# Optimization experiments

Hardware: AMD Instinct MI355X
Metric: run time of the kernel (lower is better)

## Reference

```python
import jax, jax.numpy as jnp
import numpy as np

NODES = 81
NODE_DIM = 2
IN_DIM = NODES * NODE_DIM  # 162
D = 256
H = 16
HD = D // H
DFF = 2048
T, B, E = 1024, 8, 648


def _layernorm(x, w, b, eps=1e-5):
    m = x.mean(-1, keepdims=True)
    v = x.var(-1, keepdims=True)
    return (x - m) / jnp.sqrt(v + eps) * w + b


def setup_inputs() -> dict:
    key = jax.random.key(0)
    ks = jax.random.split(key, 12)
    s = 0.02
    W = lambda k, shape: jax.random.normal(k, shape, jnp.float32) * s
    return {
        "src": jax.random.normal(ks[0], (T, B, IN_DIM), jnp.float32),
        "edge_index": jax.random.randint(ks[1], (2, E), 0, NODES),
        "gcn_w": W(ks[2], (NODE_DIM, NODE_DIM)),
        "gcn_b": jnp.zeros((NODE_DIM,), jnp.float32),
        "fc_w": W(ks[3], (IN_DIM, D)),
        "fc_b": jnp.zeros((D,), jnp.float32),
        "wq": W(ks[4], (D, D)), "bq": jnp.zeros((D,), jnp.float32),
        "wk": W(ks[5], (D, D)), "bk": jnp.zeros((D,), jnp.float32),
        "wv": W(ks[6], (D, D)), "bv": jnp.zeros((D,), jnp.float32),
        "wo": W(ks[7], (D, D)), "bo": jnp.zeros((D,), jnp.float32),
        "ln1_w": jnp.ones((D,), jnp.float32), "ln1_b": jnp.zeros((D,), jnp.float32),
        "ffn_w1": W(ks[8], (D, DFF)), "ffn_b1": jnp.zeros((DFF,), jnp.float32),
        "ffn_w2": W(ks[9], (DFF, D)), "ffn_b2": jnp.zeros((D,), jnp.float32),
        "ln2_w": jnp.ones((D,), jnp.float32), "ln2_b": jnp.zeros((D,), jnp.float32),
        "dec_w": W(ks[10], (D, IN_DIM)), "dec_b": jnp.zeros((IN_DIM,), jnp.float32),
    }


def reference(src, edge_index, gcn_w, gcn_b, fc_w, fc_b, wq, bq, wk, bk, wv, bv,
              wo, bo, ln1_w, ln1_b, ffn_w1, ffn_b1, ffn_w2, ffn_b2, ln2_w, ln2_b,
              dec_w, dec_b):
    t, b, _ = src.shape
    # ---- batched GCNConv(2,2): all T*B tiny graphs share one adjacency ----
    # src[t,b] = [in_flow(81), out_flow(81)] -> node features [81, 2]
    xg = jnp.swapaxes(src.reshape(t, b, NODE_DIM, NODES), -1, -2)  # [T,B,81,2]
    row, col = edge_index[0], edge_index[1]
    A = jnp.zeros((NODES, NODES), src.dtype).at[col, row].add(1.0)
    A = A + jnp.eye(NODES, dtype=src.dtype)          # add self-loops
    deg = A.sum(1)
    dinv = jnp.where(deg > 0, 1.0 / jnp.sqrt(deg), 0.0)
    A_hat = dinv[:, None] * A * dinv[None, :]        # D^-1/2 (A+I) D^-1/2
    hg = jnp.einsum('ij,tbjc->tbic', A_hat, xg @ gcn_w) + gcn_b  # [T,B,81,2]
    # gcn_output.transpose(0,1).view(-1): channel-major flatten
    src2 = jnp.swapaxes(hg, -1, -2).reshape(t, b, IN_DIM)
    # ---- fc + positional encoding ----
    x = src2 @ fc_w + fc_b  # [T,B,D]
    pos = jnp.arange(t, dtype=jnp.float32)[:, None]
    div = jnp.exp(jnp.arange(0, D, 2, dtype=jnp.float32) * (-np.log(10000.0) / D))
    pe = jnp.zeros((t, D), x.dtype).at[:, 0::2].set(jnp.sin(pos * div))
    pe = pe.at[:, 1::2].set(jnp.cos(pos * div))
    x = x + pe[:, None, :]
    # ---- TransformerEncoderLayer (post-norm, relu, causal mask, eval) ----
    q = (x @ wq + bq).reshape(t, b, H, HD)
    k = (x @ wk + bk).reshape(t, b, H, HD)
    v = (x @ wv + bv).reshape(t, b, H, HD)
    scores = jnp.einsum('tbhd,sbhd->bhts', q, k) / jnp.sqrt(jnp.asarray(HD, x.dtype))
    causal = jnp.tril(jnp.ones((t, t), bool))
    scores = jnp.where(causal, scores, jnp.finfo(x.dtype).min)
    attn = jax.nn.softmax(scores, axis=-1)
    ctx = jnp.einsum('bhts,sbhd->tbhd', attn, v).reshape(t, b, D) @ wo + bo
    x = _layernorm(x + ctx, ln1_w, ln1_b)
    ff = jax.nn.relu(x @ ffn_w1 + ffn_b1) @ ffn_w2 + ffn_b2
    x = _layernorm(x + ff, ln2_w, ln2_b)
    return x @ dec_w + dec_b  # [T,B,162]
```

## Files before the change

kernel.cpp:

```cpp
#include <hip/hip_runtime.h>
#include <math.h>

#define T_    1024
#define B_    8
#define D_    256
#define H_    16
#define HD_   16
#define DFF_  2048
#define NODES_ 81
#define INDIM_ 162
#define E_    648
#define M_    (T_*B_)

typedef __bf16 bf16x8 __attribute__((ext_vector_type(8)));
typedef float  f32x4  __attribute__((ext_vector_type(4)));
typedef unsigned short ushort_t;
typedef unsigned int   uint_t;

__device__ __forceinline__ ushort_t f2bf(float f) {
    union { float f; uint_t u; } c; c.f = f;
    uint_t u = c.u;
    uint_t r = u + 0x7fffu + ((u >> 16) & 1u);
    return (ushort_t)(r >> 16);
}

__device__ __forceinline__ bf16x8 zero8() {
    bf16x8 v;
#pragma unroll
    for (int e = 0; e < 8; e++) v[e] = (__bf16)0.0f;
    return v;
}

__device__ __forceinline__ void gload_lds16(const void* g, void* l) {
    __builtin_amdgcn_global_load_lds(
        (const __attribute__((address_space(1))) void*)g,
        (__attribute__((address_space(3))) void*)l, 16, 0, 0);
}

__global__ __launch_bounds__(256) void build_weff_fused(
        const int* __restrict__ edge, const float* __restrict__ gcn_w,
        const float* __restrict__ gcn_b, const float* __restrict__ fc_w,
        const float* __restrict__ fc_b, ushort_t* __restrict__ weffT,
        float* __restrict__ beff) {
    __shared__ float A[NODES_ * NODES_];
    __shared__ float dinv[NODES_];
    int tid = threadIdx.x;
    for (int i = tid; i < NODES_ * NODES_; i += 256) A[i] = 0.f;
    __syncthreads();
    for (int e = tid; e < E_; e += 256) {
        int r = edge[e];
        int c = edge[E_ + e];
        atomicAdd(&A[c * NODES_ + r], 1.0f);
    }
    __syncthreads();
    if (tid < NODES_) A[tid * NODES_ + tid] += 1.0f;
    __syncthreads();
    if (tid < NODES_) {
        float s = 0.f;
        for (int k = 0; k < NODES_; k++) s += A[tid * NODES_ + k];
        dinv[tid] = (s > 0.f) ? rsqrtf(s) : 0.f;
    }
    __syncthreads();

    int d = tid;
    int j = blockIdx.x;
    if (j < NODES_) {
        float s0 = 0.f, s1 = 0.f;
        for (int i = 0; i < NODES_; i++) {
            float a = dinv[i] * A[i * NODES_ + j] * dinv[j];
            s0 += a * fc_w[(0 * NODES_ + i) * D_ + d];
            s1 += a * fc_w[(1 * NODES_ + i) * D_ + d];
        }
        weffT[d * 192 + j]          = f2bf(gcn_w[0] * s0 + gcn_w[1] * s1);
        weffT[d * 192 + NODES_ + j] = f2bf(gcn_w[2] * s0 + gcn_w[3] * s1);
    } else {
        float t0 = 0.f, t1 = 0.f;
        for (int i = 0; i < NODES_; i++) {
            t0 += fc_w[(0 * NODES_ + i) * D_ + d];
            t1 += fc_w[(1 * NODES_ + i) * D_ + d];
        }
        beff[d] = fc_b[d] + gcn_b[0] * t0 + gcn_b[1] * t1;
        for (int c = INDIM_; c < 192; c++) weffT[d * 192 + c] = 0;
    }
}

__device__ __forceinline__ void trans_tile(
        const float* __restrict__ in, ushort_t* __restrict__ out,
        int K, int N, int Kp, int Np, int bx, int by) {
    __shared__ float tile[32][33];
    int k0 = bx * 32, n0 = by * 32;
    int tx = threadIdx.x & 31, ty = threadIdx.x >> 5;
#pragma unroll
    for (int i = 0; i < 4; i++) {
        int r = k0 + ty + i * 8, c = n0 + tx;
        tile[ty + i * 8][tx] = (r < K && c < N) ? in[(size_t)r * N + c] : 0.f;
    }
    __syncthreads();
#pragma unroll
    for (int i = 0; i < 4; i++) {
        int r = n0 + ty + i * 8, c = k0 + tx;
        out[(size_t)r * Kp + c] = f2bf(tile[tx][ty + i * 8]);
    }
}

__global__ __launch_bounds__(256) void prep_all(
        const float* __restrict__ wq, const float* __restrict__ wk,
        const float* __restrict__ wv, const float* __restrict__ wo,
        const float* __restrict__ dec_w, const float* __restrict__ w1,
        const float* __restrict__ w2,
        const float* __restrict__ bq, const float* __restrict__ bk,
        const float* __restrict__ bv,
        ushort_t* __restrict__ wqkvT, ushort_t* __restrict__ woT,
        ushort_t* __restrict__ dwT, ushort_t* __restrict__ w1T,
        ushort_t* __restrict__ w2T, float* __restrict__ qkvbias) {
    int bid = blockIdx.x;
    if (bid < 64)        { int l = bid;        trans_tile(wq,   wqkvT,          D_,   D_,     D_,   D_,   l & 7,  l >> 3); }
    else if (bid < 128)  { int l = bid - 64;   trans_tile(wk,   wqkvT + 65536,  D_,   D_,     D_,   D_,   l & 7,  l >> 3); }
    else if (bid < 192)  { int l = bid - 128;  trans_tile(wv,   wqkvT + 131072, D_,   D_,     D_,   D_,   l & 7,  l >> 3); }
    else if (bid < 256)  { int l = bid - 192;  trans_tile(wo,   woT,            D_,   D_,     D_,   D_,   l & 7,  l >> 3); }
    else if (bid < 320)  { int l = bid - 256;  trans_tile(dec_w, dwT,           D_,   INDIM_, D_,   D_,   l & 7,  l >> 3); }
    else if (bid < 832)  { int l = bid - 320;  trans_tile(w1,   w1T,            D_,   DFF_,   D_,   DFF_, l & 7,  l >> 3); }
    else if (bid < 1344) { int l = bid - 832;  trans_tile(w2,   w2T,            DFF_, D_,     DFF_, D_,   l & 63, l >> 6); }
    else {
        int i = (bid - 1344) * 256 + threadIdx.x;
        if (i < 768) qkvbias[i] = (i < 256) ? bq[i] : ((i < 512) ? bk[i - 256] : bv[i - 512]);
    }
}

__global__ void src_to_bf16(const float* __restrict__ src, ushort_t* __restrict__ out) {
    int r = blockIdx.x, c = threadIdx.x;
    out[(size_t)r * 192 + c] = (c < INDIM_) ? f2bf(src[(size_t)r * INDIM_ + c]) : (ushort_t)0;
}

enum { EP_PE = 0, EP_QKV = 1, EP_PLAIN = 2, EP_RELU = 3, EP_DEC = 4, EP_PART = 5 };

template <int EPI, int TM, int KS>
__global__ __launch_bounds__(256) void gemm_bf16(
        const ushort_t* __restrict__ A, const ushort_t* __restrict__ BT,
        const float* __restrict__ bias, float* __restrict__ Cf,
        ushort_t* __restrict__ Cb, int M, int N, int K) {
    __shared__ ushort_t sA[TM * 64];
    __shared__ ushort_t sB[128 * 64];
    int tid = threadIdx.x;
    int w = tid >> 6, lane = tid & 63;
    int cc = lane & 15, q = lane >> 4;
    int bm = blockIdx.y * TM, bn = blockIdx.x * 128;
    int part = (KS > 1) ? blockIdx.z : 0;
    int kbeg = part * (K / KS), kend = kbeg + K / KS;

    int srow = (lane >> 3);
    int sslot = lane & 7;

    const int NJ = (TM == 128) ? 4 : 2;
    int mbase = (TM == 128) ? ((w >> 1) * 64) : 0;
    int nbase = (TM == 128) ? ((w & 1) * 64) : (w * 32);

    f32x4 acc[4][NJ];
#pragma unroll
    for (int i = 0; i < 4; i++)
#pragma unroll
        for (int j = 0; j < NJ; j++)
#pragma unroll
            for (int e = 0; e < 4; e++) acc[i][j][e] = 0.f;

    for (int k0 = kbeg; k0 < kend; k0 += 64) {
        if (TM == 128) {
#pragma unroll
            for (int i = 0; i < 4; i++) {
                int r = w * 32 + i * 8 + srow;
                const ushort_t* ga = A + (size_t)(bm + r) * K + k0 + ((sslot ^ (r & 7)) * 8);
                gload_lds16(ga, &sA[(w * 32 + i * 8) * 64]);
            }
        } else {
#pragma unroll
            for (int i = 0; i < 2; i++) {
                int r = w * 16 + i * 8 + srow;
                const ushort_t* ga = A + (size_t)(bm + r) * K + k0 + ((sslot ^ (r & 7)) * 8);
                gload_lds16(ga, &sA[(w * 16 + i * 8) * 64]);
            }
        }
#pragma unroll
        for (int i = 0; i < 4; i++) {
            int r = w * 32 + i * 8 + srow;
            const ushort_t* gb = BT + (size_t)(bn + r) * K + k0 + ((sslot ^ (r & 7)) * 8);
            gload_lds16(gb, &sB[(w * 32 + i * 8) * 64]);
        }
        __syncthreads();
#pragma unroll
        for (int ks = 0; ks < 2; ks++) {
            bf16x8 af[4], bfr[NJ];
#pragma unroll
            for (int i = 0; i < 4; i++) {
                int m = mbase + i * 16 + cc;
                int off = m * 64 + (((ks * 4 + q) ^ (cc & 7)) * 8);
                af[i] = *(const bf16x8*)&sA[off];
            }
#pragma unroll
            for (int j = 0; j < NJ; j++) {
                int n = nbase + j * 16 + cc;
                int off = n * 64 + (((ks * 4 + q) ^ (cc & 7)) * 8);
                bfr[j] = *(const bf16x8*)&sB[off];
            }
#pragma unroll
            for (int i = 0; i < 4; i++)
#pragma unroll
                for (int j = 0; j < NJ; j++)
                    acc[i][j] = __builtin_amdgcn_mfma_f32_16x16x32_bf16(af[i], bfr[j], acc[i][j], 0, 0, 0);
        }
        __syncthreads();
    }

#pragma unroll
    for (int i = 0; i < 4; i++) {
#pragma unroll
        for (int j = 0; j < NJ; j++) {
            int col = bn + nbase + j * 16 + cc;
            float bv = 0.f;
            if (EPI == EP_DEC) bv = (col < INDIM_) ? bias[col] : 0.f;
            else if (EPI != EP_PART) bv = bias[col];
#pragma unroll
            for (int reg = 0; reg < 4; reg++) {
                int row = bm + mbase + i * 16 + q * 4 + reg;
                float v = acc[i][j][reg] + bv;
                if (EPI == EP_PE) {
                    int t = row >> 3;
                    float freq = __expf((float)(col & ~1) * (-9.210340371976184f / 256.f));
                    float ang = (float)t * freq;
                    v += (col & 1) ? __cosf(ang) : __sinf(ang);
                    Cf[(size_t)row * N + col] = v;
                    Cb[(size_t)row * N + col] = f2bf(v);
                } else if (EPI == EP_QKV) {
                    int t = row >> 3, b = row & 7;
                    int nn = col & 255, which = col >> 8;
                    int h = nn >> 4, hd = nn & 15;
                    Cb[(size_t)which * 2097152 +
                       ((size_t)((b * H_ + h) * T_ + t)) * HD_ + hd] = f2bf(v);
                } else if (EPI == EP_PLAIN) {
                    Cf[(size_t)row * N + col] = v;
                } else if (EPI == EP_RELU) {
                    v = fmaxf(v, 0.f);
                    Cb[(size_t)row * N + col] = f2bf(v);
                } else if (EPI == EP_DEC) {
                    if (col < INDIM_) Cf[(size_t)row * INDIM_ + col] = v;
                } else if (EPI == EP_PART) {
                    Cf[(size_t)part * M * N + (size_t)row * N + col] = v;
                }
            }
        }
    }
}

__global__ __launch_bounds__(256) void attn_mfma(
        const ushort_t* __restrict__ Qb, const ushort_t* __restrict__ Kb,
        const ushort_t* __restrict__ Vb, ushort_t* __restrict__ ctxb) {
    int qc = 7 - blockIdx.x;
    int bh = blockIdx.y;
    int tid = threadIdx.x;
    int w = tid >> 6, lane = tid & 63;
    int cc = lane & 15, q = lane >> 4;
    int qb0 = qc * 128;

    __shared__ ushort_t Ks[64 * 24];
    __shared__ ushort_t VTs[16 * 72];
    __shared__ ushort_t Ps[4][32 * 72];

    const ushort_t* Qp = Qb + (size_t)bh * (T_ * HD_);
    const ushort_t* Kp = Kb + (size_t)bh * (T_ * HD_);
    const ushort_t* Vp = Vb + (size_t)bh * (T_ * HD_);

    bf16x8 qf[2];
#pragma unroll
    for (int i = 0; i < 2; i++) {
        if (q < 2)
            qf[i] = *(const bf16x8*)&Qp[(size_t)(qb0 + w * 32 + i * 16 + cc) * HD_ + q * 8];
        else
            qf[i] = zero8();
    }

    bf16x8 ones;
#pragma unroll
    for (int e = 0; e < 8; e++) ones[e] = (__bf16)1.0f;

    f32x4 ot[2], ls[2];
#pragma unroll
    for (int i = 0; i < 2; i++)
#pragma unroll
        for (int e = 0; e < 4; e++) { ot[i][e] = 0.f; ls[i][e] = 0.f; }

    int ntiles = 2 * (qc + 1);
    int qmaxw = qb0 + w * 32 + 31;

    for (int kb = 0; kb < ntiles; kb++) {
        __syncthreads();
        if (tid < 128) {
            int r = tid >> 1, half = tid & 1;
            *(bf16x8*)&Ks[r * 24 + half * 8] =
                *(const bf16x8*)&Kp[(size_t)(kb * 64 + r) * HD_ + half * 8];
        } else {
            int t2 = tid - 128;
            int r = t2 >> 1, half = t2 & 1;
            bf16x8 vv = *(const bf16x8*)&Vp[(size_t)(kb * 64 + r) * HD_ + half * 8];
#pragma unroll
            for (int e = 0; e < 8; e++)
                VTs[(half * 8 + e) * 72 + r] = ((const ushort_t*)&vv)[e];
        }
        __syncthreads();
        if (kb * 64 > qmaxw) continue;

        f32x4 s[2][4];
#pragma unroll
        for (int j = 0; j < 4; j++) {
            bf16x8 kf;
            if (q < 2) kf = *(const bf16x8*)&Ks[(j * 16 + cc) * 24 + q * 8];
            else kf = zero8();
#pragma unroll
            for (int i = 0; i < 2; i++) {
                f32x4 z;
#pragma unroll
                for (int e = 0; e < 4; e++) z[e] = 0.f;
                s[i][j] = __builtin_amdgcn_mfma_f32_16x16x32_bf16(qf[i], kf, z, 0, 0, 0);
            }
        }

#pragma unroll
        for (int i = 0; i < 2; i++) {
            int qrow0 = qb0 + w * 32 + i * 16 + q * 4;
            bool needmask = (kb * 64 + 63) > (qb0 + w * 32 + i * 16);
#pragma unroll
            for (int j = 0; j < 4; j++) {
                int key = kb * 64 + j * 16 + cc;
#pragma unroll
                for (int reg = 0; reg < 4; reg++) {
                    float p = __expf(s[i][j][reg] * 0.25f);
                    if (needmask && key > qrow0 + reg) p = 0.f;
                    union { float f; uint_t u; } cv; cv.f = p;
                    Ps[w][(i * 16 + q * 4 + reg) * 72 + j * 16 + cc] =
                        (ushort_t)(cv.u >> 16);
                }
            }
        }

#pragma unroll
        for (int kk = 0; kk < 2; kk++) {
            bf16x8 vf = *(const bf16x8*)&VTs[cc * 72 + kk * 32 + q * 8];
#pragma unroll
            for (int i = 0; i < 2; i++) {
                bf16x8 pf = *(const bf16x8*)&Ps[w][(i * 16 + cc) * 72 + kk * 32 + q * 8];
                ot[i] = __builtin_amdgcn_mfma_f32_16x16x32_bf16(vf, pf, ot[i], 0, 0, 0);
                ls[i] = __builtin_amdgcn_mfma_f32_16x16x32_bf16(ones, pf, ls[i], 0, 0, 0);
            }
        }
    }

    int b = bh >> 4, h = bh & 15;
#pragma unroll
    for (int i = 0; i < 2; i++) {
        int t = qb0 + w * 32 + i * 16 + cc;
        float linv = 1.f / ls[i][0];
        ushort_t* op = ctxb + ((size_t)t * B_ + b) * D_ + h * HD_ + q * 4;
#pragma unroll
        for (int reg = 0; reg < 4; reg++)
            op[reg] = f2bf(ot[i][reg] * linv);
    }
}

template <int NP, bool HASB>
__global__ __launch_bounds__(256) void ln_kernel(
        const float* __restrict__ X, const float* __restrict__ P0,
        const float* __restrict__ P1, const float* __restrict__ RB,
        const float* __restrict__ w, const float* __restrict__ b,
        float* __restrict__ out, ushort_t* __restrict__ outb) {
    int wv = threadIdx.x >> 6, lane = threadIdx.x & 63;
    int row = blockIdx.x * 4 + wv;
    int c = lane * 4;
    const float4 x4 = *(const float4*)&X[(size_t)row * D_ + c];
    const float4 p4 = *(const float4*)&P0[(size_t)row * D_ + c];
    float v0 = x4.x + p4.x, v1 = x4.y + p4.y, v2 = x4.z + p4.z, v3 = x4.w + p4.w;
    if (NP == 2) {
        const float4 q4 = *(const float4*)&P1[(size_t)row * D_ + c];
        v0 += q4.x; v1 += q4.y; v2 += q4.z; v3 += q4.w;
    }
    if (HASB) {
        const float4 r4 = *(const float4*)&RB[c];
        v0 += r4.x; v1 += r4.y; v2 += r4.z; v3 += r4.w;
    }
    float s  = v0 + v1 + v2 + v3;
    float sq = v0 * v0 + v1 * v1 + v2 * v2 + v3 * v3;
    for (int off = 32; off; off >>= 1) {
        s  += __shfl_xor(s, off);
        sq += __shfl_xor(sq, off);
    }
    float mean = s * (1.f / 256.f);
    float var  = sq * (1.f / 256.f) - mean * mean;
    float rstd = rsqrtf(var + 1e-5f);
    float o0 = (v0 - mean) * rstd * w[c + 0] + b[c + 0];
    float o1 = (v1 - mean) * rstd * w[c + 1] + b[c + 1];
    float o2 = (v2 - mean) * rstd * w[c + 2] + b[c + 2];
    float o3 = (v3 - mean) * rstd * w[c + 3] + b[c + 3];
    float4 o; o.x = o0; o.y = o1; o.z = o2; o.w = o3;
    *(float4*)&out[(size_t)row * D_ + c] = o;
    ushort4 ob;
    ob.x = f2bf(o0); ob.y = f2bf(o1); ob.z = f2bf(o2); ob.w = f2bf(o3);
    *(ushort4*)&outb[(size_t)row * D_ + c] = ob;
}

extern "C" void kernel_launch(void* const* d_in, const int* in_sizes, int n_in,
                              void* d_out, int out_size, void* d_ws, size_t ws_size,
                              hipStream_t stream) {
    (void)in_sizes; (void)n_in; (void)out_size; (void)ws_size;
    const float* src     = (const float*)d_in[0];
    const int*   edge    = (const int*)d_in[1];
    const float* gcn_w   = (const float*)d_in[2];
    const float* gcn_b   = (const float*)d_in[3];
    const float* fc_w    = (const float*)d_in[4];
    const float* fc_b    = (const float*)d_in[5];
    const float* wq      = (const float*)d_in[6];
    const float* bq      = (const float*)d_in[7];
    const float* wk      = (const float*)d_in[8];
    const float* bk      = (const float*)d_in[9];
    const float* wv      = (const float*)d_in[10];
    const float* bv      = (const float*)d_in[11];
    const float* wo      = (const float*)d_in[12];
    const float* bo      = (const float*)d_in[13];
    const float* ln1_w   = (const float*)d_in[14];
    const float* ln1_b   = (const float*)d_in[15];
    const float* ffn_w1  = (const float*)d_in[16];
    const float* ffn_b1  = (const float*)d_in[17];
    const float* ffn_w2  = (const float*)d_in[18];
    const float* ffn_b2  = (const float*)d_in[19];
    const float* ln2_w   = (const float*)d_in[20];
    const float* ln2_b   = (const float*)d_in[21];
    const float* dec_w   = (const float*)d_in[22];
    const float* dec_b   = (const float*)d_in[23];
    float* out = (float*)d_out;

    float* ws = (float*)d_ws;
    float* beff    = ws;
    float* qkvbias = ws + 256;
    float* x0      = ws + 1024;
    float* tmp     = x0  + 2097152;
    float* tmp2    = tmp + 2097152;
    float* x1      = tmp2 + 2097152;
    float* x2s     = x1  + 2097152;
    ushort_t* ub   = (ushort_t*)(ws + 10486784);
    ushort_t* srcb = ub;
    ushort_t* x0b  = ub + 1572864;
    ushort_t* x1b  = x0b + 2097152;
    ushort_t* x2b  = x1b + 2097152;
    ushort_t* ctxb = x2b + 2097152;
    ushort_t* hb   = ctxb + 2097152;
    ushort_t* qkvb = hb + 16777216;
    ushort_t* weffT= qkvb + 6291456;
    ushort_t* wqkvT= weffT + 49152;
    ushort_t* woT  = wqkvT + 196608;
    ushort_t* w1T  = woT + 65536;
    ushort_t* w2T  = w1T + 524288;
    ushort_t* dwT  = w2T + 524288;

    build_weff_fused<<<82, 256, 0, stream>>>(edge, gcn_w, gcn_b, fc_w, fc_b, weffT, beff);
    prep_all<<<1347, 256, 0, stream>>>(wq, wk, wv, wo, dec_w, ffn_w1, ffn_w2,
                                       bq, bk, bv, wqkvT, woT, dwT, w1T, w2T, qkvbias);
    src_to_bf16<<<8192, 192, 0, stream>>>(src, srcb);

    gemm_bf16<EP_PE, 64, 1><<<dim3(2, 128), 256, 0, stream>>>(srcb, weffT, beff, x0, x0b, M_, D_, 192);
    gemm_bf16<EP_QKV, 64, 1><<<dim3(6, 128), 256, 0, stream>>>(x0b, wqkvT, qkvbias, nullptr, qkvb, M_, 768, D_);
    attn_mfma<<<dim3(8, 128), 256, 0, stream>>>(qkvb, qkvb + 2097152, qkvb + 4194304, ctxb);
    gemm_bf16<EP_PLAIN, 64, 1><<<dim3(2, 128), 256, 0, stream>>>(ctxb, woT, bo, tmp, nullptr, M_, D_, D_);
    ln_kernel<1, false><<<2048, 256, 0, stream>>>(x0, tmp, nullptr, nullptr, ln1_w, ln1_b, x1, x1b);
    gemm_bf16<EP_RELU, 128, 1><<<dim3(16, 64), 256, 0, stream>>>(x1b, w1T, ffn_b1, nullptr, hb, M_, DFF_, D_);
    gemm_bf16<EP_PART, 64, 2><<<dim3(2, 128, 2), 256, 0, stream>>>(hb, w2T, nullptr, tmp, nullptr, M_, D_, DFF_);
    ln_kernel<2, true><<<2048, 256, 0, stream>>>(x1, tmp, tmp2, ffn_b2, ln2_w, ln2_b, x2s, x2b);
    gemm_bf16<EP_DEC, 64, 1><<<dim3(2, 128), 256, 0, stream>>>(x2b, dwT, dec_b, out, nullptr, M_, D_, D_);
}
```

Measured before the change: 249.1 us.

## Merge prep kernels and keep attention probabilities in registers

Folds the GCN weight build and the src-to-bf16 conversion into the single prep_all launch, which removes two kernel launches. In attention, the score MFMA now has K and Q swapped so each lane's score registers can serve directly as the B operand of the PV MFMA. This removes the per-warp LDS round-trip for P, and K is now read straight from global memory. V is double-buffered in LDS so one sync per tile is dropped, and the context output is written as a vectorized ushort4 store. The trade-off is half-empty MFMA operands (K=16 padded to 32), twice as many PV MFMAs, and larger LDS use for the merged prep blocks, which lowers occupancy for them.

```diff
diff --git a/kernel.cpp b/kernel.cpp
--- a/kernel.cpp
+++ b/kernel.cpp
@@ -17,6 +17,8 @@
 typedef unsigned short ushort_t;
 typedef unsigned int   uint_t;
 
+union bfpack { bf16x8 v; uint_t u[4]; };
+
 __device__ __forceinline__ ushort_t f2bf(float f) {
     union { float f; uint_t u; } c; c.f = f;
     uint_t u = c.u;
@@ -24,6 +26,11 @@
     return (ushort_t)(r >> 16);
 }
 
+__device__ __forceinline__ uint_t fbits(float f) {
+    union { float f; uint_t u; } c; c.f = f;
+    return c.u;
+}
+
 __device__ __forceinline__ bf16x8 zero8() {
     bf16x8 v;
 #pragma unroll
@@ -37,57 +44,9 @@
         (__attribute__((address_space(3))) void*)l, 16, 0, 0);
 }
 
-__global__ __launch_bounds__(256) void build_weff_fused(
-        const int* __restrict__ edge, const float* __restrict__ gcn_w,
-        const float* __restrict__ gcn_b, const float* __restrict__ fc_w,
-        const float* __restrict__ fc_b, ushort_t* __restrict__ weffT,
-        float* __restrict__ beff) {
-    __shared__ float A[NODES_ * NODES_];
-    __shared__ float dinv[NODES_];
-    int tid = threadIdx.x;
-    for (int i = tid; i < NODES_ * NODES_; i += 256) A[i] = 0.f;
-    __syncthreads();
-    for (int e = tid; e < E_; e += 256) {
-        int r = edge[e];
-        int c = edge[E_ + e];
-        atomicAdd(&A[c * NODES_ + r], 1.0f);
-    }
-    __syncthreads();
-    if (tid < NODES_) A[tid * NODES_ + tid] += 1.0f;
-    __syncthreads();
-    if (tid < NODES_) {
-        float s = 0.f;
-        for (int k = 0; k < NODES_; k++) s += A[tid * NODES_ + k];
-        dinv[tid] = (s > 0.f) ? rsqrtf(s) : 0.f;
-    }
-    __syncthreads();
-
-    int d = tid;
-    int j = blockIdx.x;
-    if (j < NODES_) {
-        float s0 = 0.f, s1 = 0.f;
-        for (int i = 0; i < NODES_; i++) {
-            float a = dinv[i] * A[i * NODES_ + j] * dinv[j];
-            s0 += a * fc_w[(0 * NODES_ + i) * D_ + d];
-            s1 += a * fc_w[(1 * NODES_ + i) * D_ + d];
-        }
-        weffT[d * 192 + j]          = f2bf(gcn_w[0] * s0 + gcn_w[1] * s1);
-        weffT[d * 192 + NODES_ + j] = f2bf(gcn_w[2] * s0 + gcn_w[3] * s1);
-    } else {
-        float t0 = 0.f, t1 = 0.f;
-        for (int i = 0; i < NODES_; i++) {
-            t0 += fc_w[(0 * NODES_ + i) * D_ + d];
-            t1 += fc_w[(1 * NODES_ + i) * D_ + d];
-        }
-        beff[d] = fc_b[d] + gcn_b[0] * t0 + gcn_b[1] * t1;
-        for (int c = INDIM_; c < 192; c++) weffT[d * 192 + c] = 0;
-    }
-}
-
 __device__ __forceinline__ void trans_tile(
         const float* __restrict__ in, ushort_t* __restrict__ out,
-        int K, int N, int Kp, int Np, int bx, int by) {
-    __shared__ float tile[32][33];
+        float (*tile)[33], int K, int N, int Kp, int bx, int by) {
     int k0 = bx * 32, n0 = by * 32;
     int tx = threadIdx.x & 31, ty = threadIdx.x >> 5;
 #pragma unroll
@@ -104,32 +63,82 @@
 }
 
 __global__ __launch_bounds__(256) void prep_all(
+        const int* __restrict__ edge, const float* __restrict__ gcn_w,
+        const float* __restrict__ gcn_b, const float* __restrict__ fc_w,
+        const float* __restrict__ fc_b, const float* __restrict__ src,
         const float* __restrict__ wq, const float* __restrict__ wk,
         const float* __restrict__ wv, const float* __restrict__ wo,
         const float* __restrict__ dec_w, const float* __restrict__ w1,
         const float* __restrict__ w2,
         const float* __restrict__ bq, const float* __restrict__ bk,
         const float* __restrict__ bv,
+        ushort_t* __restrict__ weffT, float* __restrict__ beff,
+        ushort_t* __restrict__ srcb,
         ushort_t* __restrict__ wqkvT, ushort_t* __restrict__ woT,
         ushort_t* __restrict__ dwT, ushort_t* __restrict__ w1T,
         ushort_t* __restrict__ w2T, float* __restrict__ qkvbias) {
+    __shared__ float A[NODES_ * NODES_];
+    __shared__ float dinv[NODES_];
+    __shared__ float tile[32][33];
     int bid = blockIdx.x;
-    if (bid < 64)        { int l = bid;        trans_tile(wq,   wqkvT,          D_,   D_,     D_,   D_,   l & 7,  l >> 3); }
-    else if (bid < 128)  { int l = bid - 64;   trans_tile(wk,   wqkvT + 65536,  D_,   D_,     D_,   D_,   l & 7,  l >> 3); }
-    else if (bid < 192)  { int l = bid - 128;  trans_tile(wv,   wqkvT + 131072, D_,   D_,     D_,   D_,   l & 7,  l >> 3); }
-    else if (bid < 256)  { int l = bid - 192;  trans_tile(wo,   woT,            D_,   D_,     D_,   D_,   l & 7,  l >> 3); }
-    else if (bid < 320)  { int l = bid - 256;  trans_tile(dec_w, dwT,           D_,   INDIM_, D_,   D_,   l & 7,  l >> 3); }
-    else if (bid < 832)  { int l = bid - 320;  trans_tile(w1,   w1T,            D_,   DFF_,   D_,   DFF_, l & 7,  l >> 3); }
-    else if (bid < 1344) { int l = bid - 832;  trans_tile(w2,   w2T,            DFF_, D_,     DFF_, D_,   l & 63, l >> 6); }
-    else {
-        int i = (bid - 1344) * 256 + threadIdx.x;
-        if (i < 768) qkvbias[i] = (i < 256) ? bq[i] : ((i < 512) ? bk[i - 256] : bv[i - 512]);
-    }
-}
-
-__global__ void src_to_bf16(const float* __restrict__ src, ushort_t* __restrict__ out) {
-    int r = blockIdx.x, c = threadIdx.x;
-    out[(size_t)r * 192 + c] = (c < INDIM_) ? f2bf(src[(size_t)r * INDIM_ + c]) : (ushort_t)0;
+    int tid = threadIdx.x;
+    if (bid < 82) {
+        for (int i = tid; i < NODES_ * NODES_; i += 256) A[i] = 0.f;
+        __syncthreads();
+        for (int e = tid; e < E_; e += 256) {
+            int r = edge[e];
+            int c = edge[E_ + e];
+            atomicAdd(&A[c * NODES_ + r], 1.0f);
+        }
+        __syncthreads();
+        if (tid < NODES_) A[tid * NODES_ + tid] += 1.0f;
+        __syncthreads();
+        if (tid < NODES_) {
+            float s = 0.f;
+            for (int k = 0; k < NODES_; k++) s += A[tid * NODES_ + k];
+            dinv[tid] = (s > 0.f) ? rsqrtf(s) : 0.f;
+        }
+        __syncthreads();
+        int d = tid, j = bid;
+        if (j < NODES_) {
+            float s0 = 0.f, s1 = 0.f;
+            for (int i = 0; i < NODES_; i++) {
+                float a = dinv[i] * A[i * NODES_ + j] * dinv[j];
+                s0 += a * fc_w[(0 * NODES_ + i) * D_ + d];
+                s1 += a * fc_w[(1 * NODES_ + i) * D_ + d];
+            }
+            weffT[d * 192 + j]          = f2bf(gcn_w[0] * s0 + gcn_w[1] * s1);
+            weffT[d * 192 + NODES_ + j] = f2bf(gcn_w[2] * s0 + gcn_w[3] * s1);
+        } else {
+            float t0 = 0.f, t1 = 0.f;
+            for (int i = 0; i < NODES_; i++) {
+                t0 += fc_w[(0 * NODES_ + i) * D_ + d];
+                t1 += fc_w[(1 * NODES_ + i) * D_ + d];
+            }
+            beff[d] = fc_b[d] + gcn_b[0] * t0 + gcn_b[1] * t1;
+            for (int c = INDIM_; c < 192; c++) weffT[d * 192 + c] = 0;
+        }
+    } else if (bid < 1426) {
+        int l = bid - 82;
+        if (l < 64)        trans_tile(wq,    wqkvT,          tile, D_,   D_,     D_,   l & 7,  l >> 3);
+        else if (l < 128)  trans_tile(wk,    wqkvT + 65536,  tile, D_,   D_,     D_,   (l-64) & 7,  (l-64) >> 3);
+        else if (l < 192)  trans_tile(wv,    wqkvT + 131072, tile, D_,   D_,     D_,   (l-128) & 7, (l-128) >> 3);
+        else if (l < 256)  trans_tile(wo,    woT,            tile, D_,   D_,     D_,   (l-192) & 7, (l-192) >> 3);
+        else if (l < 320)  trans_tile(dec_w, dwT,            tile, D_,   INDIM_, D_,   (l-256) & 7, (l-256) >> 3);
+        else if (l < 832)  trans_tile(w1,    w1T,            tile, D_,   DFF_,   D_,   (l-320) & 7, (l-320) >> 3);
+        else               trans_tile(w2,    w2T,            tile, DFF_, D_,     DFF_, (l-832) & 63, (l-832) >> 6);
+    } else if (bid == 1426) {
+#pragma unroll
+        for (int k = 0; k < 3; k++) {
+            int i = k * 256 + tid;
+            qkvbias[i] = (i < 256) ? bq[i] : ((i < 512) ? bk[i - 256] : bv[i - 512]);
+        }
+    } else {
+        int r = bid - 1427;
+        if (tid < 192)
+            srcb[(size_t)r * 192 + tid] =
+                (tid < INDIM_) ? f2bf(src[(size_t)r * INDIM_ + tid]) : (ushort_t)0;
+    }
 }
 
 enum { EP_PE = 0, EP_QKV = 1, EP_PLAIN = 2, EP_RELU = 3, EP_DEC = 4, EP_PART = 5 };
@@ -260,9 +269,7 @@
     int cc = lane & 15, q = lane >> 4;
     int qb0 = qc * 128;
 
-    __shared__ ushort_t Ks[64 * 24];
-    __shared__ ushort_t VTs[16 * 72];
-    __shared__ ushort_t Ps[4][32 * 72];
+    __shared__ ushort_t VTs[2][16 * 72];
 
     const ushort_t* Qp = Qb + (size_t)bh * (T_ * HD_);
     const ushort_t* Kp = Kb + (size_t)bh * (T_ * HD_);
@@ -277,9 +284,9 @@
             qf[i] = zero8();
     }
 
-    bf16x8 ones;
-#pragma unroll
-    for (int e = 0; e < 8; e++) ones[e] = (__bf16)1.0f;
+    bf16x8 ones8;
+#pragma unroll
+    for (int e = 0; e < 8; e++) ones8[e] = (__bf16)1.0f;
 
     f32x4 ot[2], ls[2];
 #pragma unroll
@@ -291,18 +298,13 @@
     int qmaxw = qb0 + w * 32 + 31;
 
     for (int kb = 0; kb < ntiles; kb++) {
-        __syncthreads();
+        ushort_t* vbuf = VTs[kb & 1];
         if (tid < 128) {
             int r = tid >> 1, half = tid & 1;
-            *(bf16x8*)&Ks[r * 24 + half * 8] =
-                *(const bf16x8*)&Kp[(size_t)(kb * 64 + r) * HD_ + half * 8];
-        } else {
-            int t2 = tid - 128;
-            int r = t2 >> 1, half = t2 & 1;
             bf16x8 vv = *(const bf16x8*)&Vp[(size_t)(kb * 64 + r) * HD_ + half * 8];
 #pragma unroll
             for (int e = 0; e < 8; e++)
-                VTs[(half * 8 + e) * 72 + r] = ((const ushort_t*)&vv)[e];
+                vbuf[(half * 8 + e) * 72 + r] = ((const ushort_t*)&vv)[e];
         }
         __syncthreads();
         if (kb * 64 > qmaxw) continue;
@@ -311,43 +313,42 @@
 #pragma unroll
         for (int j = 0; j < 4; j++) {
             bf16x8 kf;
-            if (q < 2) kf = *(const bf16x8*)&Ks[(j * 16 + cc) * 24 + q * 8];
-            else kf = zero8();
+            if (q < 2)
+                kf = *(const bf16x8*)&Kp[(size_t)(kb * 64 + j * 16 + cc) * HD_ + q * 8];
+            else
+                kf = zero8();
 #pragma unroll
             for (int i = 0; i < 2; i++) {
                 f32x4 z;
 #pragma unroll
                 for (int e = 0; e < 4; e++) z[e] = 0.f;
-                s[i][j] = __builtin_amdgcn_mfma_f32_16x16x32_bf16(qf[i], kf, z, 0, 0, 0);
-            }
-        }
-
-#pragma unroll
-        for (int i = 0; i < 2; i++) {
-            int qrow0 = qb0 + w * 32 + i * 16 + q * 4;
-            bool needmask = (kb * 64 + 63) > (qb0 + w * 32 + i * 16);
-#pragma unroll
-            for (int j = 0; j < 4; j++) {
-                int key = kb * 64 + j * 16 + cc;
-#pragma unroll
-                for (int reg = 0; reg < 4; reg++) {
-                    float p = __expf(s[i][j][reg] * 0.25f);
-                    if (needmask && key > qrow0 + reg) p = 0.f;
-                    union { float f; uint_t u; } cv; cv.f = p;
-                    Ps[w][(i * 16 + q * 4 + reg) * 72 + j * 16 + cc] =
-                        (ushort_t)(cv.u >> 16);
-                }
-            }
-        }
-
-#pragma unroll
-        for (int kk = 0; kk < 2; kk++) {
-            bf16x8 vf = *(const bf16x8*)&VTs[cc * 72 + kk * 32 + q * 8];
+                s[i][j] = __builtin_amdgcn_mfma_f32_16x16x32_bf16(kf, qf[i], z, 0, 0, 0);
+            }
+        }
+
+#pragma unroll
+        for (int j = 0; j < 4; j++) {
+            bfpack af;
+            const uint_t* vt = (const uint_t*)&vbuf[cc * 72 + j * 16 + q * 4];
+            af.u[0] = vt[0]; af.u[1] = vt[1]; af.u[2] = 0u; af.u[3] = 0u;
+            int key0 = kb * 64 + j * 16 + q * 4;
 #pragma unroll
             for (int i = 0; i < 2; i++) {
-                bf16x8 pf = *(const bf16x8*)&Ps[w][(i * 16 + cc) * 72 + kk * 32 + q * 8];
-                ot[i] = __builtin_amdgcn_mfma_f32_16x16x32_bf16(vf, pf, ot[i], 0, 0, 0);
-                ls[i] = __builtin_amdgcn_mfma_f32_16x16x32_bf16(ones, pf, ls[i], 0, 0, 0);
+                int qrow = qb0 + w * 32 + i * 16 + cc;
+                float p0 = __expf(s[i][j][0] * 0.25f);
+                float p1 = __expf(s[i][j][1] * 0.25f);
+                float p2 = __expf(s[i][j][2] * 0.25f);
+                float p3 = __expf(s[i][j][3] * 0.25f);
+                if (key0 + 0 > qrow) p0 = 0.f;
+                if (key0 + 1 > qrow) p1 = 0.f;
+                if (key0 + 2 > qrow) p2 = 0.f;
+                if (key0 + 3 > qrow) p3 = 0.f;
+                bfpack pf;
+                pf.u[0] = (fbits(p0) >> 16) | (fbits(p1) & 0xffff0000u);
+                pf.u[1] = (fbits(p2) >> 16) | (fbits(p3) & 0xffff0000u);
+                pf.u[2] = 0u; pf.u[3] = 0u;
+                ot[i] = __builtin_amdgcn_mfma_f32_16x16x32_bf16(af.v, pf.v, ot[i], 0, 0, 0);
+                ls[i] = __builtin_amdgcn_mfma_f32_16x16x32_bf16(ones8, pf.v, ls[i], 0, 0, 0);
             }
         }
     }
@@ -357,10 +358,12 @@
     for (int i = 0; i < 2; i++) {
         int t = qb0 + w * 32 + i * 16 + cc;
         float linv = 1.f / ls[i][0];
-        ushort_t* op = ctxb + ((size_t)t * B_ + b) * D_ + h * HD_ + q * 4;
-#pragma unroll
-        for (int reg = 0; reg < 4; reg++)
-            op[reg] = f2bf(ot[i][reg] * linv);
+        ushort4 ov;
+        ov.x = f2bf(ot[i][0] * linv);
+        ov.y = f2bf(ot[i][1] * linv);
+        ov.z = f2bf(ot[i][2] * linv);
+        ov.w = f2bf(ot[i][3] * linv);
+        *(ushort4*)&ctxb[((size_t)t * B_ + b) * D_ + h * HD_ + q * 4] = ov;
     }
 }
 
@@ -457,10 +460,10 @@
     ushort_t* w2T  = w1T + 524288;
     ushort_t* dwT  = w2T + 524288;
 
-    build_weff_fused<<<82, 256, 0, stream>>>(edge, gcn_w, gcn_b, fc_w, fc_b, weffT, beff);
-    prep_all<<<1347, 256, 0, stream>>>(wq, wk, wv, wo, dec_w, ffn_w1, ffn_w2,
-                                       bq, bk, bv, wqkvT, woT, dwT, w1T, w2T, qkvbias);
-    src_to_bf16<<<8192, 192, 0, stream>>>(src, srcb);
+    prep_all<<<9619, 256, 0, stream>>>(edge, gcn_w, gcn_b, fc_w, fc_b, src,
+                                       wq, wk, wv, wo, dec_w, ffn_w1, ffn_w2,
+                                       bq, bk, bv, weffT, beff, srcb,
+                                       wqkvT, woT, dwT, w1T, w2T, qkvbias);
 
     gemm_bf16<EP_PE, 64, 1><<<dim3(2, 128), 256, 0, stream>>>(srcb, weffT, beff, x0, x0b, M_, D_, 192);
     gemm_bf16<EP_QKV, 64, 1><<<dim3(6, 128), 256, 0, stream>>>(x0b, wqkvT, qkvbias, nullptr, qkvb, M_, 768, D_);
```

After: 256.2 us. 2.9% more time.
